# Performance work log

Measured on AMD Instinct MI355X. Metric: run time of the kernel, lower is better.

Reference implementation:

```python
import jax, jax.numpy as jnp
import numpy as np

HIDDEN_DIM = 64
VOCAB_SIZE = 64
MEMORY_SLOTS = 8
SEQ_LEN = 32
B = 32768


def setup_inputs() -> dict:
    key = jax.random.key(0)
    ks = jax.random.split(key, 11)
    s = 0.1
    return {
        "seqs": jax.random.randint(ks[0], (B, SEQ_LEN), 0, VOCAB_SIZE),
        "query_tok": jax.random.randint(ks[1], (B,), 0, VOCAB_SIZE),
        "embed_table": jax.random.normal(ks[2], (VOCAB_SIZE + 2, HIDDEN_DIM), jnp.float32) * s,
        "sc_w1": jax.random.normal(ks[3], (HIDDEN_DIM, 32), jnp.float32) * s,
        "sc_b1": jax.random.normal(ks[4], (32,), jnp.float32) * s,
        "sc_w2": jax.random.normal(ks[5], (32, 1), jnp.float32) * s,
        "sc_b2": jax.random.normal(ks[6], (1,), jnp.float32) * s,
        "rh_w1": jax.random.normal(ks[7], (2 * HIDDEN_DIM, HIDDEN_DIM), jnp.float32) * s,
        "rh_b1": jax.random.normal(ks[8], (HIDDEN_DIM,), jnp.float32) * s,
        "rh_w2": jax.random.normal(ks[9], (HIDDEN_DIM, VOCAB_SIZE), jnp.float32) * s,
        "rh_b2": jax.random.normal(ks[10], (VOCAB_SIZE,), jnp.float32) * s,
    }


def reference(seqs, query_tok, embed_table, sc_w1, sc_b1, sc_w2, sc_b2,
              rh_w1, rh_b1, rh_w2, rh_b2):
    # Embed the first SEQ_LEN-1 tokens: [B, 31, H]
    embs = embed_table[seqs[:, : SEQ_LEN - 1]]
    slot_ids = jnp.arange(MEMORY_SLOTS)

    def scan_one(embs_b):
        def step(carry, emb):
            mem, count = carry  # mem: [8, H], count: scalar int32
            # score all slots (harmless during fill phase; only used when full)
            scores = (jnp.maximum(mem @ sc_w1 + sc_b1, 0.0) @ sc_w2 + sc_b2)[:, 0]
            evict_idx = jnp.argmin(scores)
            # full: pop evict_idx (shift left above it), append new emb at slot 7
            rolled = jnp.roll(mem, -1, axis=0)
            full_mem = jnp.where(slot_ids[:, None] < evict_idx, mem, rolled)
            full_mem = full_mem.at[MEMORY_SLOTS - 1].set(emb)
            # filling: write new emb at position `count`
            fill_mem = mem.at[jnp.clip(count, 0, MEMORY_SLOTS - 1)].set(emb)
            new_mem = jnp.where(count >= MEMORY_SLOTS, full_mem, fill_mem)
            new_count = jnp.minimum(count + 1, MEMORY_SLOTS)
            return (new_mem, new_count), None

        init = (jnp.zeros((MEMORY_SLOTS, HIDDEN_DIM), embs_b.dtype),
                jnp.array(0, jnp.int32))
        (mem, _), _ = jax.lax.scan(step, init, embs_b)
        return mem.mean(0)  # memory is always full (31 tokens > 8 slots)

    mem_summary = jax.vmap(scan_one)(embs)  # [B, H]
    q_emb = embed_table[query_tok]          # [B, H]
    h = jnp.concatenate([q_emb, mem_summary], axis=-1)  # [B, 2H]
    return jnp.maximum(h @ rh_w1 + rh_b1, 0.0) @ rh_w2 + rh_b2  # [B, VOCAB]
```

## Files before the change

### kernel.cpp

```cpp
#include <hip/hip_runtime.h>


#define SEQ_LEN 32
#define MEM_SLOTS 8

#define WS_SCORE 0
#define WS_Q1B   64
#define WS_M1T   (64 + 4096)

__global__ __launch_bounds__(256) void lem_precompute(
    const float* __restrict__ embed,
    const float* __restrict__ sc_w1, const float* __restrict__ sc_b1,
    const float* __restrict__ sc_w2, const float* __restrict__ sc_b2,
    const float* __restrict__ rh_w1, const float* __restrict__ rh_b1,
    float* __restrict__ ws)
{
    const int t = threadIdx.x;
    if (blockIdx.x < 16) {
        const int p = blockIdx.x * 256 + t;
        const int v = p >> 6, k = p & 63;
        const float* e = embed + v * 64;
        float q = rh_b1[k];
        float m = 0.f;
        #pragma unroll 8
        for (int i = 0; i < 64; ++i) {
            q = fmaf(e[i], rh_w1[i * 64 + k], q);
            m = fmaf(e[i], rh_w1[(64 + i) * 64 + k], m);
        }
        ws[WS_Q1B + v * 64 + k] = q;
        ws[WS_M1T + k * 64 + v] = m * 0.125f;
    } else {
        __shared__ float part[2048];
        #pragma unroll
        for (int r = 0; r < 8; ++r) {
            const int s = r * 256 + t;
            const int v = s >> 5, k = s & 31;
            const float* e = embed + v * 64;
            float a = sc_b1[k];
            #pragma unroll 8
            for (int i = 0; i < 64; ++i) a = fmaf(e[i], sc_w1[i * 32 + k], a);
            a = fmaxf(a, 0.f);
            part[s] = a * sc_w2[k];
        }
        __syncthreads();
        if (t < 64) {
            float s = sc_b2[0];
            for (int k = 0; k < 32; ++k) s += part[t * 32 + k];
            ws[WS_SCORE + t] = s;
        }
    }
}

__global__ __launch_bounds__(256) void lem_main(
    const int* __restrict__ seqs, const int* __restrict__ qtok,
    const float* __restrict__ rh_w2, const float* __restrict__ rh_b2,
    const float* __restrict__ ws, float* __restrict__ out)
{
    __shared__ float MT[4096];
    __shared__ float score_s[64];
    __shared__ unsigned long long tok_s[64];
    __shared__ float hh[4096];

    const int t = threadIdx.x;
    const int gbase = blockIdx.x * 64;

    for (int i = t; i < 4096; i += 256) MT[i] = ws[WS_M1T + i];
    if (t < 64) score_s[t] = ws[WS_SCORE + t];
    __syncthreads();

    if (t < 64) {
        const int b = gbase + t;
        int tk[SEQ_LEN];
        const int4* sq4 = (const int4*)(seqs + (long long)b * SEQ_LEN);
        #pragma unroll
        for (int r = 0; r < SEQ_LEN / 4; ++r) {
            int4 v = sq4[r];
            tk[r * 4 + 0] = v.x; tk[r * 4 + 1] = v.y;
            tk[r * 4 + 2] = v.z; tk[r * 4 + 3] = v.w;
        }
        int tok[MEM_SLOTS]; float sc[MEM_SLOTS];
        #pragma unroll
        for (int j = 0; j < MEM_SLOTS; ++j) tok[j] = tk[j];
        #pragma unroll
        for (int j = 0; j < MEM_SLOTS; ++j) sc[j] = score_s[tok[j]];
        #pragma unroll
        for (int step = MEM_SLOTS; step < SEQ_LEN - 1; ++step) {
            const int nt = tk[step];
            const float ns = score_s[nt];
            float bv = sc[0]; int be = 0;
            #pragma unroll
            for (int j = 1; j < MEM_SLOTS; ++j) {
                const bool lt = sc[j] < bv;
                bv = lt ? sc[j] : bv;
                be = lt ? j : be;
            }
            #pragma unroll
            for (int j = 0; j < MEM_SLOTS - 1; ++j) {
                const bool take = (j >= be);
                sc[j]  = take ? sc[j + 1]  : sc[j];
                tok[j] = take ? tok[j + 1] : tok[j];
            }
            sc[MEM_SLOTS - 1] = ns;
            tok[MEM_SLOTS - 1] = nt;
        }
        unsigned long long pk = 0ull;
        #pragma unroll
        for (int j = 0; j < MEM_SLOTS; ++j)
            pk |= (unsigned long long)(tok[j] & 255) << (8 * j);
        tok_s[t] = pk;
    }
    __syncthreads();

    const int lane = t & 63;
    const int w = t >> 6;
    const int k0 = w * 16;
    const int b = lane;
    const int qb = qtok[gbase + b];
    const unsigned long long pk = tok_s[b];

    float acc[16];
    {
        const float4* Q4 = (const float4*)(ws + WS_Q1B);
        const int qbase = (qb * 64 + k0) >> 2;
        #pragma unroll
        for (int j4 = 0; j4 < 4; ++j4) {
            float4 v = Q4[qbase + j4];
            acc[j4 * 4 + 0] = v.x; acc[j4 * 4 + 1] = v.y;
            acc[j4 * 4 + 2] = v.z; acc[j4 * 4 + 3] = v.w;
        }
    }
    #pragma unroll
    for (int j = 0; j < MEM_SLOTS; ++j) {
        const int tkn = (int)((pk >> (8 * j)) & 255);
        #pragma unroll
        for (int jj = 0; jj < 16; ++jj)
            acc[jj] += MT[(k0 + jj) * 64 + tkn];
    }
    #pragma unroll
    for (int jj = 0; jj < 16; ++jj)
        hh[(k0 + jj) * 64 + b] = fmaxf(acc[jj], 0.f);
    __syncthreads();

    const int m0 = __builtin_amdgcn_readfirstlane(k0);
    float o[16];
    #pragma unroll
    for (int j = 0; j < 16; ++j) o[j] = rh_b2[m0 + j];
    #pragma unroll 4
    for (int k = 0; k < 64; ++k) {
        const float h = hh[k * 64 + b];
        #pragma unroll
        for (int j = 0; j < 16; ++j)
            o[j] = fmaf(h, rh_w2[k * 64 + m0 + j], o[j]);
    }
    float4* op4 = (float4*)(out + (long long)(gbase + b) * 64 + m0);
    #pragma unroll
    for (int j4 = 0; j4 < 4; ++j4)
        op4[j4] = make_float4(o[j4 * 4 + 0], o[j4 * 4 + 1],
                              o[j4 * 4 + 2], o[j4 * 4 + 3]);
}

extern "C" void kernel_launch(void* const* d_in, const int* in_sizes, int n_in,
                              void* d_out, int out_size, void* d_ws, size_t ws_size,
                              hipStream_t stream)
{
    const int*   seqs   = (const int*)d_in[0];
    const int*   qtok   = (const int*)d_in[1];
    const float* embed  = (const float*)d_in[2];
    const float* sc_w1  = (const float*)d_in[3];
    const float* sc_b1  = (const float*)d_in[4];
    const float* sc_w2  = (const float*)d_in[5];
    const float* sc_b2  = (const float*)d_in[6];
    const float* rh_w1  = (const float*)d_in[7];
    const float* rh_b1  = (const float*)d_in[8];
    const float* rh_w2  = (const float*)d_in[9];
    const float* rh_b2  = (const float*)d_in[10];
    float* out = (float*)d_out;
    float* ws  = (float*)d_ws;

    const int B = in_sizes[1];

    lem_precompute<<<17, 256, 0, stream>>>(embed, sc_w1, sc_b1, sc_w2, sc_b2,
                                           rh_w1, rh_b1, ws);
    lem_main<<<B / 64, 256, 0, stream>>>(seqs, qtok, rh_w2, rh_b2, ws, out);
}
```

Baseline: 101.5 us.

## Compute output projection with bf16 MFMA and overlap MT staging with eviction scan

Pre-packs rh_w2 into bf16 MFMA B-fragment layout in the precompute kernel. The final 64x64 projection now runs as 32x32x16 bf16 MFMA on packed hidden activations instead of scalar FMAs over fp32 weights. It also lets waves 1-3 copy MT into shared memory with float4 loads while wave 0 runs the eviction scan, rather than serialising the two. This trades fp32 accuracy for bf16 in the output GEMM. Output stores become 4-byte strided writes instead of float4 rows.

After: 95.20 us. 1.07x faster.

```diff
diff --git a/kernel.cpp b/kernel.cpp
--- a/kernel.cpp
+++ b/kernel.cpp
@@ -7,12 +7,22 @@
 #define WS_SCORE 0
 #define WS_Q1B   64
 #define WS_M1T   (64 + 4096)
+#define WS_W2B   (64 + 4096 + 4096)
+
+typedef __attribute__((ext_vector_type(8)))  short short8;
+typedef __attribute__((ext_vector_type(16))) float floatx16;
+
+__device__ __forceinline__ uint32_t bf16rtne(float f) {
+    uint32_t u = __float_as_uint(f);
+    return (u + 0x7FFFu + ((u >> 16) & 1u)) >> 16;
+}
 
 __global__ __launch_bounds__(256) void lem_precompute(
     const float* __restrict__ embed,
     const float* __restrict__ sc_w1, const float* __restrict__ sc_b1,
     const float* __restrict__ sc_w2, const float* __restrict__ sc_b2,
     const float* __restrict__ rh_w1, const float* __restrict__ rh_b1,
+    const float* __restrict__ rh_w2,
     float* __restrict__ ws)
 {
     const int t = threadIdx.x;
@@ -42,6 +52,20 @@
             a = fmaxf(a, 0.f);
             part[s] = a * sc_w2[k];
         }
+        uint32_t* wb = (uint32_t*)ws + WS_W2B;
+        #pragma unroll
+        for (int r = 0; r < 8; ++r) {
+            const int sidx = r * 256 + t;
+            const int d = sidx & 3;
+            const int ln = (sidx >> 2) & 63;
+            const int tile = sidx >> 8;
+            const int ktile = tile >> 1, tn = tile & 1;
+            const int k = ktile * 16 + (ln >> 5) * 8 + 2 * d;
+            const int n = tn * 32 + (ln & 31);
+            const uint32_t lo = bf16rtne(rh_w2[k * 64 + n]);
+            const uint32_t hi = bf16rtne(rh_w2[(k + 1) * 64 + n]);
+            wb[sidx] = lo | (hi << 16);
+        }
         __syncthreads();
         if (t < 64) {
             float s = sc_b2[0];
@@ -53,23 +77,33 @@
 
 __global__ __launch_bounds__(256) void lem_main(
     const int* __restrict__ seqs, const int* __restrict__ qtok,
-    const float* __restrict__ rh_w2, const float* __restrict__ rh_b2,
+    const float* __restrict__ rh_b2,
     const float* __restrict__ ws, float* __restrict__ out)
 {
     __shared__ float MT[4096];
     __shared__ float score_s[64];
     __shared__ unsigned long long tok_s[64];
-    __shared__ float hh[4096];
+    __shared__ uint32_t hh2[32 * 64];
 
     const int t = threadIdx.x;
     const int gbase = blockIdx.x * 64;
-
-    for (int i = t; i < 4096; i += 256) MT[i] = ws[WS_M1T + i];
-    if (t < 64) score_s[t] = ws[WS_SCORE + t];
-    __syncthreads();
-
-    if (t < 64) {
-        const int b = gbase + t;
+    const int lane = t & 63;
+    const int w = t >> 6;
+    const int col = t & 31;
+    const int half = (t >> 5) & 1;
+    const int tile_n = w & 1;
+    const int tile_m = w >> 1;
+
+    uint4 bq[4];
+    const uint4* B4 = (const uint4*)((const uint32_t*)ws + WS_W2B);
+    #pragma unroll
+    for (int kt = 0; kt < 4; ++kt)
+        bq[kt] = B4[(kt * 2 + tile_n) * 64 + lane];
+    const float bias = rh_b2[tile_n * 32 + col];
+
+    if (w == 0) {
+        score_s[lane] = ws[WS_SCORE + lane];
+        const int b = gbase + lane;
         int tk[SEQ_LEN];
         const int4* sq4 = (const int4*)(seqs + (long long)b * SEQ_LEN);
         #pragma unroll
@@ -107,14 +141,16 @@
         #pragma unroll
         for (int j = 0; j < MEM_SLOTS; ++j)
             pk |= (unsigned long long)(tok[j] & 255) << (8 * j);
-        tok_s[t] = pk;
+        tok_s[lane] = pk;
+    } else {
+        const float4* src = (const float4*)(ws + WS_M1T);
+        float4* dst = (float4*)MT;
+        for (int i = t - 64; i < 1024; i += 192) dst[i] = src[i];
     }
     __syncthreads();
 
-    const int lane = t & 63;
-    const int w = t >> 6;
+    const int b = lane;
     const int k0 = w * 16;
-    const int b = lane;
     const int qb = qtok[gbase + b];
     const unsigned long long pk = tok_s[b];
 
@@ -137,26 +173,35 @@
             acc[jj] += MT[(k0 + jj) * 64 + tkn];
     }
     #pragma unroll
-    for (int jj = 0; jj < 16; ++jj)
-        hh[(k0 + jj) * 64 + b] = fmaxf(acc[jj], 0.f);
+    for (int j = 0; j < 8; ++j) {
+        const uint32_t lo = bf16rtne(fmaxf(acc[2 * j + 0], 0.f));
+        const uint32_t hi = bf16rtne(fmaxf(acc[2 * j + 1], 0.f));
+        hh2[(w * 8 + j) * 64 + b] = lo | (hi << 16);
+    }
     __syncthreads();
 
-    const int m0 = __builtin_amdgcn_readfirstlane(k0);
-    float o[16];
-    #pragma unroll
-    for (int j = 0; j < 16; ++j) o[j] = rh_b2[m0 + j];
-    #pragma unroll 4
-    for (int k = 0; k < 64; ++k) {
-        const float h = hh[k * 64 + b];
-        #pragma unroll
-        for (int j = 0; j < 16; ++j)
-            o[j] = fmaf(h, rh_w2[k * 64 + m0 + j], o[j]);
-    }
-    float4* op4 = (float4*)(out + (long long)(gbase + b) * 64 + m0);
-    #pragma unroll
-    for (int j4 = 0; j4 < 4; ++j4)
-        op4[j4] = make_float4(o[j4 * 4 + 0], o[j4 * 4 + 1],
-                              o[j4 * 4 + 2], o[j4 * 4 + 3]);
+    floatx16 oacc;
+    #pragma unroll
+    for (int i = 0; i < 16; ++i) oacc[i] = bias;
+
+    union U8 { uint32_t u[4]; short8 s; };
+    #pragma unroll
+    for (int kt = 0; kt < 4; ++kt) {
+        U8 a;
+        #pragma unroll
+        for (int d = 0; d < 4; ++d)
+            a.u[d] = hh2[(kt * 8 + half * 4 + d) * 64 + (tile_m * 32 + col)];
+        U8 bb;
+        bb.u[0] = bq[kt].x; bb.u[1] = bq[kt].y;
+        bb.u[2] = bq[kt].z; bb.u[3] = bq[kt].w;
+        oacc = __builtin_amdgcn_mfma_f32_32x32x16_bf16(a.s, bb.s, oacc, 0, 0, 0);
+    }
+
+    #pragma unroll
+    for (int reg = 0; reg < 16; ++reg) {
+        const int row = (reg & 3) + 8 * (reg >> 2) + 4 * half;
+        out[(long long)(gbase + tile_m * 32 + row) * 64 + tile_n * 32 + col] = oacc[reg];
+    }
 }
 
 extern "C" void kernel_launch(void* const* d_in, const int* in_sizes, int n_in,
@@ -180,6 +225,6 @@
     const int B = in_sizes[1];
 
     lem_precompute<<<17, 256, 0, stream>>>(embed, sc_w1, sc_b1, sc_w2, sc_b2,
-                                           rh_w1, rh_b1, ws);
-    lem_main<<<B / 64, 256, 0, stream>>>(seqs, qtok, rh_w2, rh_b2, ws, out);
-}
+                                           rh_w1, rh_b1, rh_w2, ws);
+    lem_main<<<B / 64, 256, 0, stream>>>(seqs, qtok, rh_b2, ws, out);
+}
```
